# Optimization experiments

Measured on AMD Instinct MI355X. Metric: run time of the kernel, lower is better.

The kernel has to match this reference:

```python
import jax, jax.numpy as jnp
import numpy as np

N = 100000
IN_F = 165
HID = 128
E = 1600000


def gcn_conv(x, W, b, src, dst, n):
    # PyG GCNConv: h = x @ W; add self-loops; symmetric norm D^-1/2 A D^-1/2; aggregate; + bias
    h = x @ W  # [n, out]
    src_sl = jnp.concatenate([src, jnp.arange(n)])
    dst_sl = jnp.concatenate([dst, jnp.arange(n)])
    deg = jax.ops.segment_sum(jnp.ones_like(src_sl, dtype=h.dtype), dst_sl, num_segments=n)
    dinv = jnp.where(deg > 0, jax.lax.rsqrt(deg), 0.0)
    norm = dinv[src_sl] * dinv[dst_sl]  # [e+n]
    msg = h[src_sl] * norm[:, None]
    out = jax.ops.segment_sum(msg, dst_sl, num_segments=n)
    return out + b


def setup_inputs() -> dict:
    key = jax.random.key(0)
    k = jax.random.split(key, 8)
    x = jax.random.normal(k[0], (N, IN_F), dtype=jnp.float32)
    edge_index = jax.random.randint(k[1], (2, E), 0, N)
    s1 = 1.0 / np.sqrt(IN_F)
    s2 = 1.0 / np.sqrt(HID)
    W1 = jax.random.uniform(k[2], (IN_F, HID), jnp.float32, -s1, s1)
    b1 = jnp.zeros((HID,), jnp.float32)
    W2 = jax.random.uniform(k[3], (HID, HID), jnp.float32, -s2, s2)
    b2 = jnp.zeros((HID,), jnp.float32)
    Wc = jax.random.uniform(k[4], (HID, 2), jnp.float32, -s2, s2)
    bc = jax.random.uniform(k[5], (2,), jnp.float32, -s2, s2)
    return {"x": x, "edge_index": edge_index, "W1": W1, "b1": b1,
            "W2": W2, "b2": b2, "Wc": Wc, "bc": bc}


def reference(x, edge_index, W1, b1, W2, b2, Wc, bc):
    src, dst = edge_index[0], edge_index[1]
    h = jax.nn.relu(gcn_conv(x, W1, b1, src, dst, N))
    # dropout inactive (eval mode)
    h = jax.nn.relu(gcn_conv(h, W2, b2, src, dst, N))
    return h @ Wc + bc
```

## Files before the change

### kernel.cpp

```cpp
#include <hip/hip_runtime.h>


typedef _Float16 half8 __attribute__((ext_vector_type(8)));
typedef float floatx4 __attribute__((ext_vector_type(4)));
typedef float f4u __attribute__((ext_vector_type(4), aligned(4)));

#define SLOT_C 64
#define BCAP 4608
#define NBKT 391
#define CHUNK 4096

__global__ __launch_bounds__(256) void multisplit_k(const int* __restrict__ src,
                                                    const int* __restrict__ dst, int e,
                                                    int* __restrict__ bcnt,
                                                    int2* __restrict__ edges2) {
  __shared__ int lhist[NBKT];
  __shared__ int lbase[NBKT];
  __shared__ int lcur[NBKT];
  int t = threadIdx.x;
  int e0 = blockIdx.x * CHUNK;
  int e1 = min(e0 + CHUNK, e);
  for (int b = t; b < NBKT; b += 256) { lhist[b] = 0; lcur[b] = 0; }
  __syncthreads();
  for (int i = e0 + t; i < e1; i += 256)
    atomicAdd(&lhist[dst[i] >> 8], 1);
  __syncthreads();
  for (int b = t; b < NBKT; b += 256) {
    int h = lhist[b];
    lbase[b] = h ? atomicAdd(&bcnt[b], h) : 0;
  }
  __syncthreads();
  for (int i = e0 + t; i < e1; i += 256) {
    int d = dst[i];
    int b = d >> 8;
    int p = lbase[b] + atomicAdd(&lcur[b], 1);
    if (p < BCAP) edges2[(size_t)b * BCAP + p] = make_int2(src[i], d);
  }
}

__global__ __launch_bounds__(256) void csr_from_bins_k(const int2* __restrict__ edges2,
                                                       const int* __restrict__ bcnt,
                                                       int* __restrict__ cnt_g,
                                                       int* __restrict__ csr,
                                                       float* __restrict__ dinv, int n) {
  __shared__ int lcnt[256];
  int b = blockIdx.x;
  int node0 = b << 8;
  int t = threadIdx.x;
  lcnt[t] = 0;
  __syncthreads();
  int ec = min(bcnt[b], BCAP);
  const int2* ebase = edges2 + (size_t)b * BCAP;
  for (int i = t; i < ec; i += 256) {
    int2 ed = ebase[i];
    int p = atomicAdd(&lcnt[ed.y - node0], 1);
    if (p < SLOT_C) csr[((size_t)ed.y << 6) + p] = ed.x;
  }
  __syncthreads();
  int node = node0 + t;
  if (node < n) {
    int c = lcnt[t];
    cnt_g[node] = c;
    dinv[node] = rsqrtf((float)(c + 1));
  }
}

__global__ void w_split_frag_k(const float* __restrict__ W, int K, int nslab,
                               _Float16* __restrict__ WF) {
  int idx = blockIdx.x * blockDim.x + threadIdx.x;
  if (idx >= nslab * 8192) return;
  int j = idx & 7;
  int lane = (idx >> 3) & 63;
  int p = (idx >> 9) & 1;
  int c = (idx >> 10) & 7;
  int s = idx >> 13;
  int k = (s << 5) + ((lane >> 4) << 3) + j;
  int col = (c << 4) + (lane & 15);
  float v = (k < K) ? W[(size_t)k * 128 + col] : 0.f;
  _Float16 h = (_Float16)v;
  WF[idx] = p ? (_Float16)(v - (float)h) : h;
}

template <bool AHALF, int NSLAB>
__global__ __launch_bounds__(256) void gemm_f16_k(const void* __restrict__ Av,
                                                  const _Float16* __restrict__ WF,
                                                  const float* __restrict__ rowscale,
                                                  _Float16* __restrict__ out,
                                                  int n, int K) {
  int wave = threadIdx.x >> 6, lane = threadIdx.x & 63;
  int m = lane & 15, quad = lane >> 4;
  int rowbase = blockIdx.x * 128 + wave * 32;
  int ra[2];
  ra[0] = min(rowbase + m, n - 1);
  ra[1] = min(rowbase + 16 + m, n - 1);

  floatx4 acc[2][8];
#pragma unroll
  for (int t = 0; t < 2; ++t)
#pragma unroll
    for (int c = 0; c < 8; ++c) acc[t][c] = (floatx4){0.f, 0.f, 0.f, 0.f};

  f4u xb[3][2][2];
  half8 hb[3][2];

  auto loadA = [&](int s, int b) {
    int k0 = (s << 5) + quad * 8;
#pragma unroll
    for (int t = 0; t < 2; ++t) {
      if constexpr (AHALF) {
        const _Float16* arow = (const _Float16*)Av + (size_t)ra[t] * K;
        hb[b][t] = *(const half8*)(arow + k0);
      } else {
        const float* arow = (const float*)Av + (size_t)ra[t] * K;
        if ((s << 5) + 32 <= K) {
          xb[b][t][0] = *(const f4u*)(arow + k0);
          xb[b][t][1] = *(const f4u*)(arow + k0 + 4);
        } else {
#pragma unroll
          for (int j = 0; j < 4; ++j) { int kk = k0 + j;     kk = kk < K ? kk : K - 1; xb[b][t][0][j] = arow[kk]; }
#pragma unroll
          for (int j = 0; j < 4; ++j) { int kk = k0 + 4 + j; kk = kk < K ? kk : K - 1; xb[b][t][1][j] = arow[kk]; }
        }
      }
    }
  };

  loadA(0, 0);
  if (NSLAB > 1) loadA(1, 1);

#pragma unroll
  for (int s = 0; s < NSLAB; ++s) {
    const _Float16* wbase = WF + (size_t)s * 8192;
    half8 wh[8], wl[8];
#pragma unroll
    for (int c = 0; c < 8; ++c) {
      wh[c] = *(const half8*)(wbase + c * 1024 + lane * 8);
      wl[c] = *(const half8*)(wbase + c * 1024 + 512 + lane * 8);
    }
    if (s + 2 < NSLAB) loadA(s + 2, (s + 2) % 3);

    int b = s % 3;
    half8 ah[2], al[2];
#pragma unroll
    for (int t = 0; t < 2; ++t) {
      if constexpr (AHALF) {
        ah[t] = hb[b][t];
      } else {
#pragma unroll
        for (int j = 0; j < 8; ++j) {
          float v = (j < 4) ? xb[b][t][0][j] : xb[b][t][1][j - 4];
          _Float16 hh = (_Float16)v;
          ah[t][j] = hh;
          al[t][j] = (_Float16)(v - (float)hh);
        }
      }
    }
#pragma unroll
    for (int c = 0; c < 8; ++c)
#pragma unroll
      for (int t = 0; t < 2; ++t) {
        acc[t][c] = __builtin_amdgcn_mfma_f32_16x16x32_f16(ah[t], wh[c], acc[t][c], 0, 0, 0);
        acc[t][c] = __builtin_amdgcn_mfma_f32_16x16x32_f16(ah[t], wl[c], acc[t][c], 0, 0, 0);
        if constexpr (!AHALF)
          acc[t][c] = __builtin_amdgcn_mfma_f32_16x16x32_f16(al[t], wh[c], acc[t][c], 0, 0, 0);
      }
  }

#pragma unroll
  for (int t = 0; t < 2; ++t) {
#pragma unroll
    for (int i = 0; i < 4; ++i) {
      int row = rowbase + t * 16 + quad * 4 + i;
      if (row < n) {
        float di = rowscale ? rowscale[row] : 1.0f;
#pragma unroll
        for (int c = 0; c < 8; ++c)
          out[(size_t)row * 128 + c * 16 + m] = (_Float16)(acc[t][c][i] * di);
      }
    }
  }
}

template <bool CLS>
__global__ __launch_bounds__(256) void aggregate_k(const _Float16* __restrict__ g,
                                                   const int* __restrict__ cnt,
                                                   const int* __restrict__ csr,
                                                   const float* __restrict__ dinv,
                                                   const float* __restrict__ bias,
                                                   const float* __restrict__ Wc,
                                                   const float* __restrict__ bc,
                                                   _Float16* __restrict__ out16,
                                                   float* __restrict__ out32, int n) {
  int wave = threadIdx.x >> 6;
  int lane = threadIdx.x & 63;
  int i = blockIdx.x * 4 + wave;
  if (i >= n) return;
  int qtr = lane >> 4;
  int l16 = lane & 15;
  int f = l16 * 8;

  float acc[8];
#pragma unroll
  for (int j = 0; j < 8; ++j) acc[j] = 0.f;

  int deg = min(cnt[i], SLOT_C);
  size_t s0 = (size_t)i << 6;

  if (deg > 0) {
    int last = deg - 1;
    for (int eb = 0; eb < deg; eb += 16) {
#pragma unroll
      for (int k = 0; k < 4; ++k) {
        int ee = eb + 4 * k + qtr;
        float w = (ee <= last) ? 1.f : 0.f;
        int ec = (ee <= last) ? ee : last;
        int srow = csr[s0 + ec];
        half8 v = *(const half8*)&g[(size_t)srow * 128 + f];
#pragma unroll
        for (int j = 0; j < 8; ++j) acc[j] = fmaf(w, (float)v[j], acc[j]);
      }
    }
#pragma unroll
    for (int j = 0; j < 8; ++j) {
      acc[j] += __shfl_xor(acc[j], 16, 64);
      acc[j] += __shfl_xor(acc[j], 32, 64);
    }
  }

  half8 self = *(const half8*)&g[(size_t)i * 128 + f];
  float di = dinv[i];
  float4 b0 = *(const float4*)&bias[f];
  float4 b1 = *(const float4*)&bias[f + 4];
  float bv[8] = {b0.x, b0.y, b0.z, b0.w, b1.x, b1.y, b1.z, b1.w};
  float r[8];
#pragma unroll
  for (int j = 0; j < 8; ++j)
    r[j] = fmaxf((acc[j] + (float)self[j]) * di + bv[j], 0.f);

  if (!CLS) {
    if (qtr == 0) {
      half8 o;
#pragma unroll
      for (int j = 0; j < 8; ++j) o[j] = (_Float16)(r[j] * di);
      *(half8*)&out16[(size_t)i * 128 + f] = o;
    }
  } else {
    float c0v = 0.f, c1v = 0.f;
#pragma unroll
    for (int q = 0; q < 4; ++q) {
      float4 wv = *(const float4*)&Wc[f * 2 + q * 4];
      c0v += r[q * 2] * wv.x + r[q * 2 + 1] * wv.z;
      c1v += r[q * 2] * wv.y + r[q * 2 + 1] * wv.w;
    }
#pragma unroll
    for (int off = 8; off > 0; off >>= 1) {
      c0v += __shfl_down(c0v, off, 16);
      c1v += __shfl_down(c1v, off, 16);
    }
    if (lane == 0) {
      out32[(size_t)i * 2 + 0] = c0v + bc[0];
      out32[(size_t)i * 2 + 1] = c1v + bc[1];
    }
  }
}

extern "C" void kernel_launch(void* const* d_in, const int* in_sizes, int n_in,
                              void* d_out, int out_size, void* d_ws, size_t ws_size,
                              hipStream_t stream) {
  const float* x  = (const float*)d_in[0];
  const int*   ei = (const int*)d_in[1];
  const float* W1 = (const float*)d_in[2];
  const float* b1 = (const float*)d_in[3];
  const float* W2 = (const float*)d_in[4];
  const float* b2 = (const float*)d_in[5];
  const float* Wc = (const float*)d_in[6];
  const float* bc = (const float*)d_in[7];
  float* out = (float*)d_out;

  const int IN_F = 165;
  const int NS1 = 6;
  const int NS2 = 4;
  const int n = in_sizes[0] / IN_F;
  const int e = in_sizes[1] / 2;
  const int* src = ei;
  const int* dst = ei + e;

  char* ws = (char*)d_ws;
  size_t off = 0;
  auto alloc = [&](size_t bytes) -> void* {
    void* p = ws + off;
    off += (bytes + 255) & ~(size_t)255;
    return p;
  };
  _Float16* bufA = (_Float16*)alloc((size_t)n * 128 * 2);
  _Float16* bufB = (_Float16*)alloc((size_t)n * 128 * 2);
  int*   csr  = (int*)alloc((size_t)n * SLOT_C * 4);
  int2*  edges2 = (int2*)alloc((size_t)NBKT * BCAP * 8);
  int*   cnt  = (int*)alloc((size_t)n * 4);
  int*   bcnt = (int*)alloc((size_t)NBKT * 4);
  float* dinv = (float*)alloc((size_t)n * 4);
  _Float16* wf1 = (_Float16*)alloc((size_t)NS1 * 8192 * 2);
  _Float16* wf2 = (_Float16*)alloc((size_t)NS2 * 8192 * 2);

  hipMemsetAsync(bcnt, 0, (size_t)NBKT * 4, stream);

  w_split_frag_k<<<NS1 * 32, 256, 0, stream>>>(W1, IN_F, NS1, wf1);
  w_split_frag_k<<<NS2 * 32, 256, 0, stream>>>(W2, 128, NS2, wf2);

  multisplit_k<<<(e + CHUNK - 1) / CHUNK, 256, 0, stream>>>(src, dst, e, bcnt, edges2);
  csr_from_bins_k<<<NBKT, 256, 0, stream>>>(edges2, bcnt, cnt, csr, dinv, n);

  const int gemmgrid = (n + 127) / 128;
  gemm_f16_k<false, NS1><<<gemmgrid, 256, 0, stream>>>(x, wf1, dinv, bufA, n, IN_F);
  aggregate_k<false><<<(n + 3) / 4, 256, 0, stream>>>(bufA, cnt, csr, dinv, b1, nullptr, nullptr,
                                                      bufB, nullptr, n);
  gemm_f16_k<true, NS2><<<gemmgrid, 256, 0, stream>>>(bufB, wf2, nullptr, bufA, n, 128);
  aggregate_k<true><<<(n + 3) / 4, 256, 0, stream>>>(bufA, cnt, csr, dinv, b2, Wc, bc,
                                                     nullptr, out, n);
}
```

Baseline: 338.0 us.

## Pack degree into CSR slot and load neighbor list with one wave-wide read

The per-node degree is now stored in the last slot of each node's 64-entry CSR row, which removes the separate count array. The aggregate kernel loads the whole row with one coalesced 64-lane read and hands out neighbor indices with shuffles instead of issuing dependent scalar loads per edge. The gather loop is fully unrolled into three degree buckets (16, 32 or 64 slots), which exposes more independent loads at once. The cost is one fewer neighbor slot per node (63 instead of 64), plus possible wasted masked gathers for nodes whose degree sits just past a bucket boundary.

```diff
diff --git a/kernel.cpp b/kernel.cpp
--- a/kernel.cpp
+++ b/kernel.cpp
@@ -40,7 +40,6 @@
 
 __global__ __launch_bounds__(256) void csr_from_bins_k(const int2* __restrict__ edges2,
                                                        const int* __restrict__ bcnt,
-                                                       int* __restrict__ cnt_g,
                                                        int* __restrict__ csr,
                                                        float* __restrict__ dinv, int n) {
   __shared__ int lcnt[256];
@@ -54,13 +53,13 @@
   for (int i = t; i < ec; i += 256) {
     int2 ed = ebase[i];
     int p = atomicAdd(&lcnt[ed.y - node0], 1);
-    if (p < SLOT_C) csr[((size_t)ed.y << 6) + p] = ed.x;
+    if (p < SLOT_C - 1) csr[((size_t)ed.y << 6) + p] = ed.x;
   }
   __syncthreads();
   int node = node0 + t;
   if (node < n) {
     int c = lcnt[t];
-    cnt_g[node] = c;
+    csr[((size_t)node << 6) + (SLOT_C - 1)] = c;
     dinv[node] = rsqrtf((float)(c + 1));
   }
 }
@@ -183,7 +182,6 @@
 
 template <bool CLS>
 __global__ __launch_bounds__(256) void aggregate_k(const _Float16* __restrict__ g,
-                                                   const int* __restrict__ cnt,
                                                    const int* __restrict__ csr,
                                                    const float* __restrict__ dinv,
                                                    const float* __restrict__ bias,
@@ -199,38 +197,47 @@
   int l16 = lane & 15;
   int f = l16 * 8;
 
-  float acc[8];
-#pragma unroll
-  for (int j = 0; j < 8; ++j) acc[j] = 0.f;
-
-  int deg = min(cnt[i], SLOT_C);
-  size_t s0 = (size_t)i << 6;
-
-  if (deg > 0) {
-    int last = deg - 1;
-    for (int eb = 0; eb < deg; eb += 16) {
-#pragma unroll
-      for (int k = 0; k < 4; ++k) {
-        int ee = eb + 4 * k + qtr;
-        float w = (ee <= last) ? 1.f : 0.f;
-        int ec = (ee <= last) ? ee : last;
-        int srow = csr[s0 + ec];
-        half8 v = *(const half8*)&g[(size_t)srow * 128 + f];
-#pragma unroll
-        for (int j = 0; j < 8; ++j) acc[j] = fmaf(w, (float)v[j], acc[j]);
-      }
-    }
-#pragma unroll
-    for (int j = 0; j < 8; ++j) {
-      acc[j] += __shfl_xor(acc[j], 16, 64);
-      acc[j] += __shfl_xor(acc[j], 32, 64);
-    }
-  }
-
+  int sv = csr[((size_t)i << 6) + lane];
   half8 self = *(const half8*)&g[(size_t)i * 128 + f];
   float di = dinv[i];
   float4 b0 = *(const float4*)&bias[f];
   float4 b1 = *(const float4*)&bias[f + 4];
+
+  int deg = min(__shfl(sv, SLOT_C - 1, 64), SLOT_C - 1);
+
+  float acc[8];
+#pragma unroll
+  for (int j = 0; j < 8; ++j) acc[j] = 0.f;
+
+  auto grp = [&](int k) {
+    int ee = 4 * k + qtr;
+    bool valid = ee < deg;
+    int ec = valid ? ee : 0;
+    int srow = __shfl(sv, ec, 64);
+    half8 v = *(const half8*)&g[(size_t)srow * 128 + f];
+    float w = valid ? 1.f : 0.f;
+#pragma unroll
+    for (int j = 0; j < 8; ++j) acc[j] = fmaf(w, (float)v[j], acc[j]);
+  };
+
+  if (deg > 0) {
+    if (deg <= 16) {
+#pragma unroll
+      for (int k = 0; k < 4; ++k) grp(k);
+    } else if (deg <= 32) {
+#pragma unroll
+      for (int k = 0; k < 8; ++k) grp(k);
+    } else {
+#pragma unroll
+      for (int k = 0; k < 16; ++k) grp(k);
+    }
+#pragma unroll
+    for (int j = 0; j < 8; ++j) {
+      acc[j] += __shfl_xor(acc[j], 16, 64);
+      acc[j] += __shfl_xor(acc[j], 32, 64);
+    }
+  }
+
   float bv[8] = {b0.x, b0.y, b0.z, b0.w, b1.x, b1.y, b1.z, b1.w};
   float r[8];
 #pragma unroll
@@ -296,7 +303,6 @@
   _Float16* bufB = (_Float16*)alloc((size_t)n * 128 * 2);
   int*   csr  = (int*)alloc((size_t)n * SLOT_C * 4);
   int2*  edges2 = (int2*)alloc((size_t)NBKT * BCAP * 8);
-  int*   cnt  = (int*)alloc((size_t)n * 4);
   int*   bcnt = (int*)alloc((size_t)NBKT * 4);
   float* dinv = (float*)alloc((size_t)n * 4);
   _Float16* wf1 = (_Float16*)alloc((size_t)NS1 * 8192 * 2);
@@ -308,13 +314,13 @@
   w_split_frag_k<<<NS2 * 32, 256, 0, stream>>>(W2, 128, NS2, wf2);
 
   multisplit_k<<<(e + CHUNK - 1) / CHUNK, 256, 0, stream>>>(src, dst, e, bcnt, edges2);
-  csr_from_bins_k<<<NBKT, 256, 0, stream>>>(edges2, bcnt, cnt, csr, dinv, n);
+  csr_from_bins_k<<<NBKT, 256, 0, stream>>>(edges2, bcnt, csr, dinv, n);
 
   const int gemmgrid = (n + 127) / 128;
   gemm_f16_k<false, NS1><<<gemmgrid, 256, 0, stream>>>(x, wf1, dinv, bufA, n, IN_F);
-  aggregate_k<false><<<(n + 3) / 4, 256, 0, stream>>>(bufA, cnt, csr, dinv, b1, nullptr, nullptr,
+  aggregate_k<false><<<(n + 3) / 4, 256, 0, stream>>>(bufA, csr, dinv, b1, nullptr, nullptr,
                                                       bufB, nullptr, n);
   gemm_f16_k<true, NS2><<<gemmgrid, 256, 0, stream>>>(bufB, wf2, nullptr, bufA, n, 128);
-  aggregate_k<true><<<(n + 3) / 4, 256, 0, stream>>>(bufA, cnt, csr, dinv, b2, Wc, bc,
+  aggregate_k<true><<<(n + 3) / 4, 256, 0, stream>>>(bufA, csr, dinv, b2, Wc, bc,
                                                      nullptr, out, n);
 }
```

Result: no change. 342.2 us (+1.2%).
